# Kernel optimization log

Hardware: AMD Instinct MI355X
Metric: run time of the kernel (lower is better)

Reference implementation:

```python
import jax, jax.numpy as jnp
import numpy as np

ALPHA = 0.2        # LeakyReLU negative slope (config['alpha'])
NEG_INF = -9e15    # mask value from the original code


def setup_inputs() -> dict:
    key = jax.random.key(0)
    k1, k2, k3, k4 = jax.random.split(key, 4)
    N, Fin, Fout = 8192, 512, 256
    inp = jax.random.normal(k1, (N, Fin), dtype=jnp.float32)
    adj = jax.random.randint(k2, (N, N), 0, 2, dtype=jnp.int32)
    # xavier_uniform with gain=1.414
    limW = 1.414 * np.sqrt(6.0 / (Fin + Fout))
    W = jax.random.uniform(k3, (Fin, Fout), dtype=jnp.float32, minval=-limW, maxval=limW)
    lima = 1.414 * np.sqrt(6.0 / (2 * Fout + 1))
    a = jax.random.uniform(k4, (2 * Fout, 1), dtype=jnp.float32, minval=-lima, maxval=lima)
    return {"input": inp, "adj": adj, "W": W, "a": a}


def reference(input, adj, W, a):
    # h: [N, F]
    h = input @ W
    Fout = W.shape[1]
    # The original builds a_input[i, j] = concat(h_i, h_j) and dots with a.
    # Equivalently: e_ij = leakyrelu(h_i . a[:F] + h_j . a[F:]), computed
    # without the O(N^2 * 2F) intermediate.
    s1 = h @ a[:Fout, 0]   # [N] contribution from node i
    s2 = h @ a[Fout:, 0]   # [N] contribution from node j
    e = s1[:, None] + s2[None, :]                     # [N, N]
    e = jnp.where(e > 0, e, ALPHA * e)                # LeakyReLU
    scores = jnp.where(adj > 0, e, NEG_INF)
    attention = jax.nn.softmax(scores, axis=1)        # row-wise softmax
    # dropout is identity in inference mode (training=False)
    h_prime = attention @ h                           # [N, F]
    return jax.nn.elu(h_prime)                        # concat=True path
```

## Files before the change

### kernel.cpp

```cpp
#include <hip/hip_runtime.h>
#include <stdint.h>
#include <stddef.h>


#define N_NODES 8192
#define FIN     512
#define FOUT    256
#define LRALPHA 0.2f
#define MI_SHIFT 16.0f

typedef float f32x4 __attribute__((ext_vector_type(4)));
typedef short s16x8 __attribute__((ext_vector_type(8)));
typedef unsigned short u16x4 __attribute__((ext_vector_type(4)));
typedef int   i32x4 __attribute__((ext_vector_type(4)));
typedef unsigned long long u64;

typedef const uint32_t __attribute__((address_space(1)))* gas1_u32;
typedef uint32_t __attribute__((address_space(3)))* las3_u32;

__device__ __forceinline__ short f2bf_rne(float f) {
  uint32_t u = __builtin_bit_cast(uint32_t, f);
  u += 0x7fffu + ((u >> 16) & 1u);
  return (short)(u >> 16);
}
__device__ __forceinline__ short f2bf_fast(float f) {
  uint32_t u = __builtin_bit_cast(uint32_t, f);
  return (short)((u + 0x8000u) >> 16);
}
__device__ __forceinline__ float bf2f(short s) {
  uint32_t u = ((uint32_t)(uint16_t)s) << 16;
  return __builtin_bit_cast(float, u);
}

__global__ __launch_bounds__(256) void k_prep(const float* __restrict__ W,
                                              uint16_t* __restrict__ WThi,
                                              uint16_t* __restrict__ WTlo) {
  const int idx = blockIdx.x * 256 + threadIdx.x;
  const int n = idx >> 9;
  const int k = idx & 511;
  float v = W[k * FOUT + n];
  short h = f2bf_rne(v);
  WThi[idx] = (uint16_t)h;
  WTlo[idx] = (uint16_t)f2bf_rne(v - bf2f(h));
}

__global__ __launch_bounds__(256, 4) void k_pre(const float* __restrict__ X,
                                                const uint16_t* __restrict__ WThi,
                                                const uint16_t* __restrict__ WTlo,
                                                const float* __restrict__ a,
                                                uint16_t* __restrict__ HTf,
                                                float* __restrict__ s1g,
                                                float* __restrict__ s2g) {
  __shared__ float ls1[16], ls2[16];
  __shared__ uint16_t tile[FOUT * 16];
  const int lane = threadIdx.x & 63;
  const int w    = threadIdx.x >> 6;

  const int m    = lane & 15;
  const int quad = lane >> 4;
  const int i0   = blockIdx.x * 16;
  const int colg = w * 64;

  f32x4 acc[4];
#pragma unroll
  for (int cb = 0; cb < 4; ++cb) { f32x4 z = {0.f,0.f,0.f,0.f}; acc[cb] = z; }

  for (int kt = 0; kt < FIN / 32; ++kt) {
    const int k0 = kt * 32 + quad * 8;
    const float* ap = X + (size_t)(i0 + m) * FIN + k0;
    f32x4 a0 = *(const f32x4*)ap;
    f32x4 a1 = *(const f32x4*)(ap + 4);
    s16x8 ahi, alo;
#pragma unroll
    for (int e = 0; e < 4; ++e) {
      short h0 = f2bf_rne(a0[e]); ahi[e] = h0; alo[e] = f2bf_rne(a0[e] - bf2f(h0));
      short h1 = f2bf_rne(a1[e]); ahi[4+e] = h1; alo[4+e] = f2bf_rne(a1[e] - bf2f(h1));
    }
#pragma unroll
    for (int cb = 0; cb < 4; ++cb) {
      const int n = colg + cb * 16 + m;
      s16x8 bhi = *(const s16x8*)(WThi + (size_t)n * FIN + k0);
      s16x8 blo = *(const s16x8*)(WTlo + (size_t)n * FIN + k0);
      acc[cb] = __builtin_amdgcn_mfma_f32_16x16x32_bf16(ahi, bhi, acc[cb], 0, 0, 0);
      acc[cb] = __builtin_amdgcn_mfma_f32_16x16x32_bf16(ahi, blo, acc[cb], 0, 0, 0);
      acc[cb] = __builtin_amdgcn_mfma_f32_16x16x32_bf16(alo, bhi, acc[cb], 0, 0, 0);
    }
  }

  float p1[4] = {0.f,0.f,0.f,0.f}, p2[4] = {0.f,0.f,0.f,0.f};
#pragma unroll
  for (int cb = 0; cb < 4; ++cb) {
    const int n = colg + cb * 16 + m;
    const float a1c = a[n];
    const float a2c = a[FOUT + n];
#pragma unroll
    for (int reg = 0; reg < 4; ++reg) {
      p1[reg] += acc[cb][reg] * a1c;
      p2[reg] += acc[cb][reg] * a2c;
    }
  }
#pragma unroll
  for (int off = 1; off <= 8; off <<= 1)
#pragma unroll
    for (int reg = 0; reg < 4; ++reg) {
      p1[reg] += __shfl_xor(p1[reg], off);
      p2[reg] += __shfl_xor(p2[reg], off);
    }
  if (threadIdx.x < 16) { ls1[threadIdx.x] = 0.f; ls2[threadIdx.x] = 0.f; }
  __syncthreads();
  if (m == 0) {
#pragma unroll
    for (int reg = 0; reg < 4; ++reg) {
      atomicAdd(&ls1[quad * 4 + reg], p1[reg]);
      atomicAdd(&ls2[quad * 4 + reg], p2[reg]);
    }
  }
#pragma unroll
  for (int cb = 0; cb < 4; ++cb) {
    const int col = colg + cb * 16 + m;
    u16x4 pk;
#pragma unroll
    for (int reg = 0; reg < 4; ++reg) pk[reg] = (uint16_t)f2bf_rne(acc[cb][reg]);
    *(u16x4*)(tile + col * 16 + quad * 4) = pk;
  }
  __syncthreads();
  const int t = threadIdx.x;
  if (t < 16) { s1g[i0 + t] = ls1[t]; s2g[i0 + t] = ls2[t]; }
  const int jt = i0 >> 5;
  const int qh = (i0 >> 4) & 1;
  const int c  = t >> 4;
  const int mm = t & 15;
#pragma unroll
  for (int qq = 0; qq < 2; ++qq) {
    uint4 v = *(const uint4*)(tile + (c * 16 + mm) * 16 + qq * 8);
    *(uint4*)(HTf + ((((size_t)jt * 16 + c) * 64) + (qh * 2 + qq) * 16 + mm) * 8) = v;
  }
}

__global__ __launch_bounds__(512, 4) void k_attn(const uint16_t* __restrict__ HTf,
                                                 const float* __restrict__ s1,
                                                 const float* __restrict__ s2,
                                                 const int* __restrict__ adj,
                                                 float* __restrict__ pout,
                                                 float* __restrict__ pden,
                                                 int split) {
  __shared__ uint16_t PL[2][2048];
  __shared__ uint16_t BL[2][8192];
  __shared__ float lss2[1024];

  const int tid  = threadIdx.x;
  const int lane = tid & 63;
  const int w    = tid >> 6;
  const int m    = lane & 15;
  const int q    = lane >> 4;
  const int rg   = w >> 2, cg = w & 3;
  const int rr   = tid >> 3;
  const int cw   = tid & 7;
  const int i0   = blockIdx.x * 64;
  const int sp   = blockIdx.y;
  const int jrange = N_NODES / split;
  const int jbeg   = sp * jrange;
  const int jblk   = jbeg >> 5;
  const int nphase = jrange / 32;

  const float s1r = s1[i0 + rr];
  float mi = fmaxf(s1r + MI_SHIFT, LRALPHA * (s1r + MI_SHIFT));

  f32x4 acc[2][4];
#pragma unroll
  for (int rt = 0; rt < 2; ++rt)
#pragma unroll
    for (int cb = 0; cb < 4; ++cb) { f32x4 z = {0.f,0.f,0.f,0.f}; acc[rt][cb] = z; }
  float den = 0.f;

  const int* adjp = adj + (size_t)(i0 + rr) * N_NODES + jbeg + cw * 4;
  i32x4 A0 = *(const i32x4*)adjp;
  i32x4 A1 = *(const i32x4*)(adjp + 32);

#define STAGE_B(pp, buf) do {                                                  \
    const uint16_t* s_ = HTf + (((size_t)(jblk + (pp))) << 13) + (w << 10) +   \
                         (lane << 3);                                          \
    __builtin_amdgcn_global_load_lds((gas1_u32)(const void*)s_,                \
        (las3_u32)(void*)(&BL[buf][w << 10]), 16, 0, 0);                       \
    __builtin_amdgcn_global_load_lds((gas1_u32)(const void*)(s_ + 512),        \
        (las3_u32)(void*)(&BL[buf][(w << 10) + 512]), 16, 0, 0);               \
  } while (0)

  STAGE_B(0, 0);

#pragma unroll 1
  for (int p = 0; p < nphase; ++p) {
    if ((p & 31) == 0) {
      __syncthreads();
      if (tid < 256) *(f32x4*)(lss2 + tid * 4) =
        *(const f32x4*)(s2 + jbeg + (p >> 5) * 1024 + tid * 4);
      __syncthreads();
    }
    const int pl = p & 31;
    f32x4 sA = *(const f32x4*)(lss2 + pl * 32 + cw * 4);
    u16x4 P0;
#pragma unroll
    for (int e = 0; e < 4; ++e) {
      float x0 = s1r + sA[e];
      float pv0 = __expf(fmaxf(x0, LRALPHA * x0) - mi);
      pv0 = A0[e] ? pv0 : 0.f;
      den += pv0; P0[e] = (uint16_t)f2bf_fast(pv0);
    }
    *(u16x4*)(PL[p & 1] + (((cw >> 1) * 64 + rr) * 8) + (cw & 1) * 4) = P0;
    __syncthreads();
    i32x4 A2 = {0,0,0,0};
    if (p + 2 < nphase) A2 = *(const i32x4*)(adjp + (size_t)(p + 2) * 32);
    if (p + 1 < nphase) STAGE_B(p + 1, (p + 1) & 1);
    s16x8 F[2];
#pragma unroll
    for (int rt = 0; rt < 2; ++rt)
      F[rt] = *(const s16x8*)(PL[p & 1] + (q * 64 + rg * 32 + rt * 16 + m) * 8);
    __builtin_amdgcn_s_setprio(1);
#pragma unroll
    for (int cb = 0; cb < 4; ++cb) {
      s16x8 Bv = *(const s16x8*)(&BL[p & 1][((cg * 4 + cb) << 9) + (lane << 3)]);
#pragma unroll
      for (int rt = 0; rt < 2; ++rt)
        acc[rt][cb] = __builtin_amdgcn_mfma_f32_16x16x32_bf16(Bv, F[rt], acc[rt][cb], 0, 0, 0);
    }
    __builtin_amdgcn_s_setprio(0);
    A0 = A1; A1 = A2;
  }
#undef STAGE_B

  den += __shfl_xor(den, 1);
  den += __shfl_xor(den, 2);
  den += __shfl_xor(den, 4);
  if (cw == 0) pden[(size_t)sp * N_NODES + i0 + rr] = den;

#pragma unroll
  for (int rt = 0; rt < 2; ++rt)
#pragma unroll
    for (int cb = 0; cb < 4; ++cb) {
      const int row = i0 + rg * 32 + rt * 16 + m;
      const int col = cg * 64 + cb * 16 + q * 4;
      *(f32x4*)(pout + ((size_t)sp * N_NODES + row) * FOUT + col) = acc[rt][cb];
    }
}

__global__ __launch_bounds__(256) void k_reduce(const float* __restrict__ pout,
                                                const float* __restrict__ pden,
                                                float* __restrict__ out,
                                                int split) {
  const int gid = blockIdx.x * 256 + threadIdx.x;
  const int i = gid >> 6;
  const int c = (gid & 63) << 2;
  f32x4 sum = {0.f,0.f,0.f,0.f};
  float den = 0.f;
  for (int s = 0; s < split; ++s) {
    sum += *(const f32x4*)(pout + ((size_t)s * N_NODES + i) * FOUT + c);
    den += pden[(size_t)s * N_NODES + i];
  }
  const float inv = 1.0f / den;
  f32x4 r;
#pragma unroll
  for (int e = 0; e < 4; ++e) {
    float v = sum[e] * inv;
    r[e] = v > 0.f ? v : (__expf(v) - 1.0f);
  }
  *(f32x4*)(out + (size_t)i * FOUT + c) = r;
}

extern "C" void kernel_launch(void* const* d_in, const int* in_sizes, int n_in,
                              void* d_out, int out_size, void* d_ws, size_t ws_size,
                              hipStream_t stream) {
  const float* X   = (const float*)d_in[0];
  const int*   adj = (const int*)d_in[1];
  const float* W   = (const float*)d_in[2];
  const float* a   = (const float*)d_in[3];
  float* out = (float*)d_out;

  char* ws = (char*)d_ws;
  uint16_t* HTf  = (uint16_t*)ws;
  uint16_t* WThi = (uint16_t*)(ws + (4u << 20));
  uint16_t* WTlo = (uint16_t*)(ws + (4u << 20) + 262144);
  float*    s1   = (float*)(ws + (4u << 20) + 524288);
  float*    s2   = s1 + N_NODES;
  float*    pden = s2 + N_NODES;
  const size_t pout_off = (size_t)16u << 20;
  const size_t slab = (size_t)N_NODES * FOUT * sizeof(float);

  int split;
  if      (ws_size >= pout_off + 4 * slab) split = 4;
  else if (ws_size >= pout_off + 2 * slab) split = 2;
  else                                     split = 1;
  float* pout = (split == 1) ? out : (float*)(ws + pout_off);

  k_prep<<<dim3(512), dim3(256), 0, stream>>>(W, WThi, WTlo);
  k_pre<<<dim3(512), dim3(256), 0, stream>>>(X, WThi, WTlo, a, HTf, s1, s2);
  k_attn<<<dim3(N_NODES / 64, split), dim3(512), 0, stream>>>(HTf, s1, s2, adj, pout, pden, split);
  k_reduce<<<dim3(N_NODES * FOUT / 4 / 256), dim3(256), 0, stream>>>(pout, pden, out, split);
}
```

Baseline: 458.7 us.

## Halve attention row tile to 32 and reduce split-K from 4 to 2

The attention kernel now processes 32 query rows per block instead of 64. Each of the 8 waves covers 32 output columns for all rows, and 16 threads per row compute 2 probabilities each. To keep the block count similar, the j-range split drops from 4 to 2, which halves partial-output traffic and reduction work. The cost is that each staged H tile is reused across half as many rows, roughly doubling HTf reads from L2 relative to MFMA work.

Measured after the change: 486.6 us. 1.06x slower.

```diff
diff --git a/kernel.cpp b/kernel.cpp
--- a/kernel.cpp
+++ b/kernel.cpp
@@ -12,7 +12,9 @@
 typedef float f32x4 __attribute__((ext_vector_type(4)));
 typedef short s16x8 __attribute__((ext_vector_type(8)));
 typedef unsigned short u16x4 __attribute__((ext_vector_type(4)));
+typedef unsigned short u16x2 __attribute__((ext_vector_type(2)));
 typedef int   i32x4 __attribute__((ext_vector_type(4)));
+typedef int   i32x2 __attribute__((ext_vector_type(2)));
 typedef unsigned long long u64;
 
 typedef const uint32_t __attribute__((address_space(1)))* gas1_u32;
@@ -144,7 +146,7 @@
                                                  float* __restrict__ pout,
                                                  float* __restrict__ pden,
                                                  int split) {
-  __shared__ uint16_t PL[2][2048];
+  __shared__ uint16_t PL[2][1024];
   __shared__ uint16_t BL[2][8192];
   __shared__ float lss2[1024];
 
@@ -153,10 +155,9 @@
   const int w    = tid >> 6;
   const int m    = lane & 15;
   const int q    = lane >> 4;
-  const int rg   = w >> 2, cg = w & 3;
-  const int rr   = tid >> 3;
-  const int cw   = tid & 7;
-  const int i0   = blockIdx.x * 64;
+  const int rr   = tid >> 4;
+  const int cw   = tid & 15;
+  const int i0   = blockIdx.x * 32;
   const int sp   = blockIdx.y;
   const int jrange = N_NODES / split;
   const int jbeg   = sp * jrange;
@@ -166,16 +167,16 @@
   const float s1r = s1[i0 + rr];
   float mi = fmaxf(s1r + MI_SHIFT, LRALPHA * (s1r + MI_SHIFT));
 
-  f32x4 acc[2][4];
+  f32x4 acc[2][2];
 #pragma unroll
   for (int rt = 0; rt < 2; ++rt)
 #pragma unroll
-    for (int cb = 0; cb < 4; ++cb) { f32x4 z = {0.f,0.f,0.f,0.f}; acc[rt][cb] = z; }
+    for (int cb = 0; cb < 2; ++cb) { f32x4 z = {0.f,0.f,0.f,0.f}; acc[rt][cb] = z; }
   float den = 0.f;
 
-  const int* adjp = adj + (size_t)(i0 + rr) * N_NODES + jbeg + cw * 4;
-  i32x4 A0 = *(const i32x4*)adjp;
-  i32x4 A1 = *(const i32x4*)(adjp + 32);
+  const int* adjp = adj + (size_t)(i0 + rr) * N_NODES + jbeg + cw * 2;
+  i32x2 A0 = *(const i32x2*)adjp;
+  i32x2 A1 = *(const i32x2*)(adjp + 32);
 
 #define STAGE_B(pp, buf) do {                                                  \
     const uint16_t* s_ = HTf + (((size_t)(jblk + (pp))) << 13) + (w << 10) +   \
@@ -197,28 +198,32 @@
       __syncthreads();
     }
     const int pl = p & 31;
-    f32x4 sA = *(const f32x4*)(lss2 + pl * 32 + cw * 4);
-    u16x4 P0;
-#pragma unroll
-    for (int e = 0; e < 4; ++e) {
-      float x0 = s1r + sA[e];
+    const float sA0 = lss2[pl * 32 + cw * 2];
+    const float sA1 = lss2[pl * 32 + cw * 2 + 1];
+    u16x2 P0;
+    {
+      float x0 = s1r + sA0;
       float pv0 = __expf(fmaxf(x0, LRALPHA * x0) - mi);
-      pv0 = A0[e] ? pv0 : 0.f;
-      den += pv0; P0[e] = (uint16_t)f2bf_fast(pv0);
-    }
-    *(u16x4*)(PL[p & 1] + (((cw >> 1) * 64 + rr) * 8) + (cw & 1) * 4) = P0;
+      pv0 = A0[0] ? pv0 : 0.f;
+      den += pv0; P0[0] = (uint16_t)f2bf_fast(pv0);
+      float x1 = s1r + sA1;
+      float pv1 = __expf(fmaxf(x1, LRALPHA * x1) - mi);
+      pv1 = A0[1] ? pv1 : 0.f;
+      den += pv1; P0[1] = (uint16_t)f2bf_fast(pv1);
+    }
+    *(u16x2*)(PL[p & 1] + (((cw >> 2) * 32 + rr) * 8) + (cw & 3) * 2) = P0;
     __syncthreads();
-    i32x4 A2 = {0,0,0,0};
-    if (p + 2 < nphase) A2 = *(const i32x4*)(adjp + (size_t)(p + 2) * 32);
+    i32x2 A2 = {0,0};
+    if (p + 2 < nphase) A2 = *(const i32x2*)(adjp + (size_t)(p + 2) * 32);
     if (p + 1 < nphase) STAGE_B(p + 1, (p + 1) & 1);
     s16x8 F[2];
 #pragma unroll
     for (int rt = 0; rt < 2; ++rt)
-      F[rt] = *(const s16x8*)(PL[p & 1] + (q * 64 + rg * 32 + rt * 16 + m) * 8);
+      F[rt] = *(const s16x8*)(PL[p & 1] + (q * 32 + rt * 16 + m) * 8);
     __builtin_amdgcn_s_setprio(1);
 #pragma unroll
-    for (int cb = 0; cb < 4; ++cb) {
-      s16x8 Bv = *(const s16x8*)(&BL[p & 1][((cg * 4 + cb) << 9) + (lane << 3)]);
+    for (int cb = 0; cb < 2; ++cb) {
+      s16x8 Bv = *(const s16x8*)(&BL[p & 1][((w * 2 + cb) << 9) + (lane << 3)]);
 #pragma unroll
       for (int rt = 0; rt < 2; ++rt)
         acc[rt][cb] = __builtin_amdgcn_mfma_f32_16x16x32_bf16(Bv, F[rt], acc[rt][cb], 0, 0, 0);
@@ -231,14 +236,15 @@
   den += __shfl_xor(den, 1);
   den += __shfl_xor(den, 2);
   den += __shfl_xor(den, 4);
+  den += __shfl_xor(den, 8);
   if (cw == 0) pden[(size_t)sp * N_NODES + i0 + rr] = den;
 
 #pragma unroll
   for (int rt = 0; rt < 2; ++rt)
 #pragma unroll
-    for (int cb = 0; cb < 4; ++cb) {
-      const int row = i0 + rg * 32 + rt * 16 + m;
-      const int col = cg * 64 + cb * 16 + q * 4;
+    for (int cb = 0; cb < 2; ++cb) {
+      const int row = i0 + rt * 16 + m;
+      const int col = w * 32 + cb * 16 + q * 4;
       *(f32x4*)(pout + ((size_t)sp * N_NODES + row) * FOUT + col) = acc[rt][cb];
     }
 }
@@ -286,13 +292,12 @@
   const size_t slab = (size_t)N_NODES * FOUT * sizeof(float);
 
   int split;
-  if      (ws_size >= pout_off + 4 * slab) split = 4;
-  else if (ws_size >= pout_off + 2 * slab) split = 2;
+  if      (ws_size >= pout_off + 2 * slab) split = 2;
   else                                     split = 1;
   float* pout = (split == 1) ? out : (float*)(ws + pout_off);
 
   k_prep<<<dim3(512), dim3(256), 0, stream>>>(W, WThi, WTlo);
   k_pre<<<dim3(512), dim3(256), 0, stream>>>(X, WThi, WTlo, a, HTf, s1, s2);
-  k_attn<<<dim3(N_NODES / 64, split), dim3(512), 0, stream>>>(HTf, s1, s2, adj, pout, pden, split);
+  k_attn<<<dim3(N_NODES / 32, split), dim3(512), 0, stream>>>(HTf, s1, s2, adj, pout, pden, split);
   k_reduce<<<dim3(N_NODES * FOUT / 4 / 256), dim3(256), 0, stream>>>(pout, pden, out, split);
 }
```
